# Kernel optimization log

Measured on AMD Instinct MI355X. Metric: run time of the kernel, lower is better.

The kernel has to match this reference:

```python
import jax, jax.numpy as jnp
import numpy as np

N_HEADS = 8
FACTOR = 5


def setup_inputs() -> dict:
    key = jax.random.key(0)
    ks = jax.random.split(key, 8)
    B, L, D = 2, 4096, 512
    sample_k = min(FACTOR * int(np.ceil(np.log(L))), L)  # 45
    inp = {
        "queries": jax.random.normal(ks[0], (B, L, D), jnp.float32),
        "keys": jax.random.normal(ks[1], (B, L, D), jnp.float32),
        "values": jax.random.normal(ks[2], (B, L, D), jnp.float32),
        "Wq": jax.random.normal(ks[3], (D, D), jnp.float32) * 0.02,
        "bq": jnp.zeros((D,), jnp.float32),
        "Wk": jax.random.normal(ks[4], (D, D), jnp.float32) * 0.02,
        "bk": jnp.zeros((D,), jnp.float32),
        "Wv": jax.random.normal(ks[5], (D, D), jnp.float32) * 0.02,
        "bv": jnp.zeros((D,), jnp.float32),
        "index_sample": jax.random.randint(ks[6], (L, sample_k), 0, L, jnp.int32),
    }
    return inp


def reference(queries, keys, values, Wq, bq, Wk, bk, Wv, bv, index_sample):
    b, l_q, d_model = queries.shape
    _, l_k, _ = keys.shape
    h = N_HEADS
    d = d_model // h
    # projections -> [b, h, l, d]
    q = (queries @ Wq + bq).reshape(b, l_q, h, d).transpose(0, 2, 1, 3)
    k = (keys @ Wk + bk).reshape(b, l_k, h, d).transpose(0, 2, 1, 3)
    v = (values @ Wv + bv).reshape(b, l_k, h, d).transpose(0, 2, 1, 3)
    n_top = min(FACTOR * int(np.ceil(np.log(l_q))), l_q)
    # --- prob_qk: sparse sampled QK ---
    # gather sampled keys per query position: [b, h, l_q, sample_k, d]
    k_sample = k[:, :, index_sample, :]
    q_k_sample = jnp.einsum('bhld,bhlsd->bhls', q, k_sample)
    # sparsity measure M(q, K) = max - mean
    m = q_k_sample.max(-1) - q_k_sample.sum(-1) / l_k  # [b, h, l_q]
    _, m_top = jax.lax.top_k(m, n_top)  # [b, h, n_top]
    q_reduce = jnp.take_along_axis(q, m_top[..., None], axis=2)  # [b, h, u, d]
    scores = jnp.einsum('bhud,bhkd->bhuk', q_reduce, k)  # [b, h, u, l_k]
    scale = float(1.0 / np.sqrt(d))
    scores = scores * scale
    # --- causal ProbMask on the selected query rows ---
    causal = jnp.triu(jnp.ones((l_q, l_k), bool), 1)
    mask = causal[m_top]  # [b, h, u, l_k]
    scores = jnp.where(mask, -jnp.inf, scores)
    attn = jax.nn.softmax(scores, axis=-1)
    # --- initial context: causal cumsum of V; scatter updated rows ---
    context = jnp.cumsum(v, axis=2)  # [b, h, l_q, d]
    upd = jnp.einsum('bhuk,bhkd->bhud', attn, v)
    bi = jnp.arange(b)[:, None, None]
    hi = jnp.arange(h)[None, :, None]
    context = context.at[bi, hi, m_top].set(upd)
    return context.transpose(0, 2, 1, 3).reshape(b, l_q, h * d)
```

## Files before the change

### kernel.cpp

```cpp
#include <hip/hip_runtime.h>
#include <math.h>

#define B  2
#define L  4096
#define D  512
#define H  8
#define DH 64
#define BH (B * H)
#define K3 1536
#define XPW 1024

typedef short s16x8 __attribute__((ext_vector_type(8)));
typedef float f32x4 __attribute__((ext_vector_type(4)));

#define AS1 __attribute__((address_space(1)))
#define AS3 __attribute__((address_space(3)))

__device__ __forceinline__ void lds_load16(const void* g, void* l) {
    __builtin_amdgcn_global_load_lds((const AS1 unsigned int*)g,
                                     (AS3 unsigned int*)l, 16, 0, 0);
}

__device__ __forceinline__ unsigned short f2bf(float x) {
    union { float f; unsigned u; } v; v.f = x;
    unsigned u = v.u;
    return (unsigned short)((u + 0x7fff + ((u >> 16) & 1)) >> 16);
}
__device__ __forceinline__ float bf2f(unsigned short h) {
    union { float f; unsigned u; } v; v.u = ((unsigned)h) << 16;
    return v.f;
}

#define MEMFENCE asm volatile("" ::: "memory")
__device__ __forceinline__ void wg_bar() {
    MEMFENCE;
    __builtin_amdgcn_s_barrier();
    MEMFENCE;
}

__global__ __launch_bounds__(256)
void k_split(const float* __restrict__ q, const float* __restrict__ k,
             const float* __restrict__ v,
             const float* __restrict__ wq, const float* __restrict__ wk,
             const float* __restrict__ wv,
             unsigned short* __restrict__ Xp, unsigned short* __restrict__ WpT)
{
    const int tid = threadIdx.x;
    if (blockIdx.x < 192) {
        __shared__ float t[64][65];
        const int bx = blockIdx.x;
        const int e  = bx >> 6;
        const int k0 = (bx & 7) * 64;
        const int n0 = ((bx >> 3) & 7) * 64;
        const float* W = (e == 0) ? wq : (e == 1) ? wk : wv;

        for (int idx = tid; idx < 64 * 16; idx += 256) {
            const int i = idx >> 4, j4 = (idx & 15) << 2;
            *(float4*)&t[i][j4] = *(const float4*)(W + (size_t)(k0 + i) * 512 + n0 + j4);
        }
        __syncthreads();

        const int n_loc = tid >> 2;
        const int kq    = (tid & 3) << 4;
        unsigned short h[16], l[16];
        #pragma unroll
        for (int tt = 0; tt < 16; tt++) {
            const float x = t[kq + tt][n_loc];
            h[tt] = f2bf(x);
            l[tt] = f2bf(x - bf2f(h[tt]));
        }
        unsigned short* base = WpT + (size_t)e * 512 * K3 + (size_t)(n0 + n_loc) * K3 + k0 + kq;
        #pragma unroll
        for (int g4 = 0; g4 < 4; g4++) {
            ushort4 hv = make_ushort4(h[g4*4], h[g4*4+1], h[g4*4+2], h[g4*4+3]);
            ushort4 lv = make_ushort4(l[g4*4], l[g4*4+1], l[g4*4+2], l[g4*4+3]);
            *(ushort4*)(base + g4*4)        = hv;
            *(ushort4*)(base + 512 + g4*4)  = lv;
        }
    } else {
        const size_t g = (size_t)(blockIdx.x - 192) * 256 + tid;
        const size_t per = (size_t)8192 * 128;
        const int e = (int)(g / per);
        const size_t rem = g - (size_t)e * per;
        const int m  = (int)(rem >> 7);
        const int kq = (int)(rem & 127) << 2;

        const float* X = (e == 0) ? q : (e == 1) ? k : v;
        const float4 x = *(const float4*)(X + (size_t)m * 512 + kq);

        unsigned short h0 = f2bf(x.x), h1 = f2bf(x.y), h2 = f2bf(x.z), h3 = f2bf(x.w);
        unsigned short* dst = Xp + (size_t)e * 8192 * XPW + (size_t)m * XPW + kq;
        *(ushort4*)(dst) = make_ushort4(h0, h1, h2, h3);
        if (e != 2) {
            unsigned short l0 = f2bf(x.x - bf2f(h0)), l1 = f2bf(x.y - bf2f(h1));
            unsigned short l2 = f2bf(x.z - bf2f(h2)), l3 = f2bf(x.w - bf2f(h3));
            *(ushort4*)(dst + 512) = make_ushort4(l0, l1, l2, l3);
        }
    }
}

#define MFMA16 __builtin_amdgcn_mfma_f32_16x16x32_bf16

__global__ __launch_bounds__(256, 2)
void gemm_mfma(const unsigned short* __restrict__ Xp,
               const unsigned short* __restrict__ WpT,
               const float* __restrict__ bq, const float* __restrict__ bk,
               const float* __restrict__ bv,
               float* __restrict__ Qo, float* __restrict__ Ko,
               float* __restrict__ Vo)
{
    __shared__ __align__(16) unsigned short lds[32768];

    const int e = blockIdx.z;
    const float* bias = (e == 0) ? bq : (e == 1) ? bk : bv;
    float* C          = (e == 0) ? Qo : (e == 1) ? Ko : Vo;
    const unsigned short* Ag = Xp  + (size_t)e * 8192 * XPW;
    const unsigned short* Bg = WpT + (size_t)e * 512 * K3;

    const int tid  = threadIdx.x;
    const int lane = tid & 63;
    const int wid  = tid >> 6;
    const int wm   = wid & 1;
    const int wn   = wid >> 1;
    const int m0   = blockIdx.x * 128;
    const int n0g  = blockIdx.y * 128;

    const int srow = lane >> 2;
    const int spos = lane & 3;
    const int sswz = (spos ^ ((srow >> 1) & 3)) << 3;
    const int row0 = wid * 32 + srow;
    const int row1 = row0 + 16;

    const unsigned short* aH0 = Ag + (size_t)(m0 + row0) * XPW + sswz;
    const unsigned short* aH1 = Ag + (size_t)(m0 + row1) * XPW + sswz;
    const unsigned short* aL0 = aH0 + 512;
    const unsigned short* aL1 = aH1 + 512;
    const unsigned short* bH0 = Bg + (size_t)(n0g + row0) * K3 + sswz;
    const unsigned short* bH1 = Bg + (size_t)(n0g + row1) * K3 + sswz;
    const unsigned short* bL0 = bH0 + 512;
    const unsigned short* bL1 = bH1 + 512;

    const int wr0 = wid * 1024;
    const int wr1 = wr0 + 512;

    const int r16 = lane & 15, quad = lane >> 4;
    const int laneOff = r16 * 64 + ((quad ^ ((r16 >> 1) & 3)) << 4);
    const char* ldsC = (const char*)lds;

    f32x4 acc[4][4];
    #pragma unroll
    for (int i = 0; i < 4; i++)
        #pragma unroll
        for (int j = 0; j < 4; j++)
            acc[i][j] = (f32x4){0.f, 0.f, 0.f, 0.f};

    const int NT = 16;

    if (e != 2) {
        #define STAGE_QK(kk, nu) do {                                   \
            const int ka_ = (kk) * 32;                                  \
            unsigned short* dd_ = lds + (nu);                           \
            lds_load16(aH0 + ka_, dd_ + wr0);                           \
            lds_load16(aH1 + ka_, dd_ + wr1);                           \
            lds_load16(aL0 + ka_, dd_ + 4096  + wr0);                   \
            lds_load16(aL1 + ka_, dd_ + 4096  + wr1);                   \
            lds_load16(bH0 + ka_, dd_ + 8192  + wr0);                   \
            lds_load16(bH1 + ka_, dd_ + 8192  + wr1);                   \
            lds_load16(bL0 + ka_, dd_ + 12288 + wr0);                   \
            lds_load16(bL1 + ka_, dd_ + 12288 + wr1);                   \
        } while (0)

        STAGE_QK(0, 0);
        s16x8 aF[4], bh[4], bl[4];

        for (int t = 0; t < NT; ++t) {
            const int pa = (t & 1) << 15;
            const int nu = (~t & 1) << 14;
            if (t + 1 < NT) {
                STAGE_QK(t + 1, nu);
                asm volatile("s_waitcnt vmcnt(8)" ::: "memory");
            } else {
                asm volatile("s_waitcnt vmcnt(0)" ::: "memory");
            }
            wg_bar();

            const char* base = ldsC + pa;
            const char* fAh = base + (wm * 64) * 64 + laneOff;
            const char* fAl = base + 8192  + (wm * 64) * 64 + laneOff;
            const char* fBh = base + 16384 + (wn * 64) * 64 + laneOff;
            const char* fBl = base + 24576 + (wn * 64) * 64 + laneOff;

            #pragma unroll
            for (int mq = 0; mq < 4; mq++) aF[mq] = *(const s16x8*)(fAh + mq * 1024);
            #pragma unroll
            for (int nq = 0; nq < 4; nq++) {
                bh[nq] = *(const s16x8*)(fBh + nq * 1024);
                bl[nq] = *(const s16x8*)(fBl + nq * 1024);
            }
            __builtin_amdgcn_s_setprio(1);
            #pragma unroll
            for (int mq = 0; mq < 4; mq++)
                #pragma unroll
                for (int nq = 0; nq < 4; nq++)
                    acc[mq][nq] = MFMA16(aF[mq], bh[nq], acc[mq][nq], 0, 0, 0);
            #pragma unroll
            for (int mq = 0; mq < 4; mq++)
                #pragma unroll
                for (int nq = 0; nq < 4; nq++)
                    acc[mq][nq] = MFMA16(aF[mq], bl[nq], acc[mq][nq], 0, 0, 0);
            __builtin_amdgcn_s_setprio(0);

            #pragma unroll
            for (int mq = 0; mq < 4; mq++) aF[mq] = *(const s16x8*)(fAl + mq * 1024);
            __builtin_amdgcn_s_setprio(1);
            #pragma unroll
            for (int mq = 0; mq < 4; mq++)
                #pragma unroll
                for (int nq = 0; nq < 4; nq++)
                    acc[mq][nq] = MFMA16(aF[mq], bh[nq], acc[mq][nq], 0, 0, 0);
            __builtin_amdgcn_s_setprio(0);
            wg_bar();
        }
    } else {
        #define STAGE_V(kk, nu) do {                                    \
            const int ka_ = (kk) * 32;                                  \
            unsigned short* dd_ = lds + (nu);                           \
            lds_load16(aH0 + ka_, dd_ + wr0);                           \
            lds_load16(aH1 + ka_, dd_ + wr1);                           \
            lds_load16(bH0 + ka_, dd_ + 8192 + wr0);                    \
            lds_load16(bH1 + ka_, dd_ + 8192 + wr1);                    \
        } while (0)

        STAGE_V(0, 0);
        s16x8 aF[4], bh[4];

        for (int t = 0; t < NT; ++t) {
            const int pa = (t & 1) << 15;
            const int nu = (~t & 1) << 14;
            if (t + 1 < NT) {
                STAGE_V(t + 1, nu);
                asm volatile("s_waitcnt vmcnt(4)" ::: "memory");
            } else {
                asm volatile("s_waitcnt vmcnt(0)" ::: "memory");
            }
            wg_bar();

            const char* base = ldsC + pa;
            const char* fAh = base + (wm * 64) * 64 + laneOff;
            const char* fBh = base + 16384 + (wn * 64) * 64 + laneOff;
            #pragma unroll
            for (int mq = 0; mq < 4; mq++) aF[mq] = *(const s16x8*)(fAh + mq * 1024);
            #pragma unroll
            for (int nq = 0; nq < 4; nq++) bh[nq] = *(const s16x8*)(fBh + nq * 1024);
            __builtin_amdgcn_s_setprio(1);
            #pragma unroll
            for (int mq = 0; mq < 4; mq++)
                #pragma unroll
                for (int nq = 0; nq < 4; nq++)
                    acc[mq][nq] = MFMA16(aF[mq], bh[nq], acc[mq][nq], 0, 0, 0);
            __builtin_amdgcn_s_setprio(0);
            wg_bar();
        }
    }

    #pragma unroll
    for (int nt = 0; nt < 4; nt++) {
        const int col = n0g + wn * 64 + nt * 16 + r16;
        const float bb = bias[col];
        #pragma unroll
        for (int mt = 0; mt < 4; mt++) {
            const int row0e = m0 + wm * 64 + mt * 16 + quad * 4;
            #pragma unroll
            for (int i = 0; i < 4; i++)
                C[(size_t)(row0e + i) * 512 + col] = acc[mt][nt][i] + bb;
        }
    }
}

#define CH 64
__global__ __launch_bounds__(256)
void k_sample_chunks(const float* __restrict__ Q, const float* __restrict__ K,
                     const int* __restrict__ idx, float* __restrict__ m_out, int S,
                     const float* __restrict__ V, float* __restrict__ partial)
{
    const int tid = threadIdx.x;
    if (blockIdx.x < 256) {
        const int bid = blockIdx.x;
        const int c  = (bid & 15) * 4 + (tid >> 6);
        const int h  = (bid >> 4) & (H - 1);
        const int b  = bid >> 7;
        const int d  = tid & 63;
        const float* base = V + (size_t)b * L * D + h * DH + d + (size_t)(c * CH) * D;

        float vals[CH];
        #pragma unroll
        for (int i = 0; i < CH; i++) vals[i] = base[(size_t)i * D];

        float s0 = 0.f, s1 = 0.f, s2 = 0.f, s3 = 0.f;
        #pragma unroll
        for (int i = 0; i < CH; i += 4) {
            s0 += vals[i]; s1 += vals[i+1]; s2 += vals[i+2]; s3 += vals[i+3];
        }
        partial[((size_t)((b * H + h) * 64 + c)) * DH + d] = (s0 + s1) + (s2 + s3);
    } else {
        const int lane = tid & 63;
        const int wib  = tid >> 6;
        const int i    = blockIdx.x - 256;
        const int bh   = i & 15;
        const int lg   = i >> 4;
        const int l = lg * 4 + wib;
        const int h = bh & (H - 1);
        const int b = bh >> 3;
        const int widx = (bh << 12) | l;

        const int r4 = lane >> 2;
        const int c4 = lane & 3;

        float4 qf[4];
        {
            const float4* qv = (const float4*)(Q + ((size_t)b * L + l) * D + h * DH);
            #pragma unroll
            for (int ii = 0; ii < 4; ii++) qf[ii] = qv[c4 + 4 * ii];
        }

        const float* Kb = K + (size_t)b * L * D + h * DH;
        const int* is = idx + (size_t)l * S;

        int  jj[3];
        bool ok[3];
        #pragma unroll
        for (int p = 0; p < 3; p++) {
            const int sp = p * 16 + r4;
            ok[p] = sp < S;
            jj[p] = ok[p] ? is[sp] : 0;
        }
        const float4* r0 = (const float4*)(Kb + (size_t)jj[0] * D);
        const float4* r1 = (const float4*)(Kb + (size_t)jj[1] * D);
        const float4* r2 = (const float4*)(Kb + (size_t)jj[2] * D);

        float4 k00 = r0[c4],     k01 = r0[c4 + 4], k02 = r0[c4 + 8], k03 = r0[c4 + 12];
        float4 k10 = r1[c4],     k11 = r1[c4 + 4], k12 = r1[c4 + 8], k13 = r1[c4 + 12];
        float4 k20 = r2[c4],     k21 = r2[c4 + 4], k22 = r2[c4 + 8], k23 = r2[c4 + 12];
        __builtin_amdgcn_sched_barrier(0);

        float vmax = -INFINITY, vsum = 0.f;
        {
            float dot = 0.f;
            dot += qf[0].x * k00.x + qf[0].y * k00.y + qf[0].z * k00.z + qf[0].w * k00.w;
            dot += qf[1].x * k01.x + qf[1].y * k01.y + qf[1].z * k01.z + qf[1].w * k01.w;
            dot += qf[2].x * k02.x + qf[2].y * k02.y + qf[2].z * k02.z + qf[2].w * k02.w;
            dot += qf[3].x * k03.x + qf[3].y * k03.y + qf[3].z * k03.z + qf[3].w * k03.w;
            dot += __shfl_xor(dot, 1, 64);
            dot += __shfl_xor(dot, 2, 64);
            if (ok[0]) { vmax = fmaxf(vmax, dot); if (c4 == 0) vsum += dot; }
        }
        {
            float dot = 0.f;
            dot += qf[0].x * k10.x + qf[0].y * k10.y + qf[0].z * k10.z + qf[0].w * k10.w;
            dot += qf[1].x * k11.x + qf[1].y * k11.y + qf[1].z * k11.z + qf[1].w * k11.w;
            dot += qf[2].x * k12.x + qf[2].y * k12.y + qf[2].z * k12.z + qf[2].w * k12.w;
            dot += qf[3].x * k13.x + qf[3].y * k13.y + qf[3].z * k13.z + qf[3].w * k13.w;
            dot += __shfl_xor(dot, 1, 64);
            dot += __shfl_xor(dot, 2, 64);
            if (ok[1]) { vmax = fmaxf(vmax, dot); if (c4 == 0) vsum += dot; }
        }
        {
            float dot = 0.f;
            dot += qf[0].x * k20.x + qf[0].y * k20.y + qf[0].z * k20.z + qf[0].w * k20.w;
            dot += qf[1].x * k21.x + qf[1].y * k21.y + qf[1].z * k21.z + qf[1].w * k21.w;
            dot += qf[2].x * k22.x + qf[2].y * k22.y + qf[2].z * k22.z + qf[2].w * k22.w;
            dot += qf[3].x * k23.x + qf[3].y * k23.y + qf[3].z * k23.z + qf[3].w * k23.w;
            dot += __shfl_xor(dot, 1, 64);
            dot += __shfl_xor(dot, 2, 64);
            if (ok[2]) { vmax = fmaxf(vmax, dot); if (c4 == 0) vsum += dot; }
        }
        #pragma unroll
        for (int off = 32; off >= 4; off >>= 1) {
            vmax = fmaxf(vmax, __shfl_xor(vmax, off, 64));
            vsum += __shfl_xor(vsum, off, 64);
        }
        if (lane == 0) m_out[widx] = vmax - vsum * (1.0f / (float)L);
    }
}

__global__ __launch_bounds__(256)
void topk_kernel(const float* __restrict__ m_in, int* __restrict__ m_top,
                 float* __restrict__ sums, int* __restrict__ flags, int NT)
{
    __shared__ unsigned hist[256];
    __shared__ unsigned sfx[257];
    __shared__ int sh_b, sh_rem;
    __shared__ int cnt_gt, cnt_eq;
    __shared__ int eqlist[128];

    const float* m = m_in + (size_t)blockIdx.x * L;
    const int tid = threadIdx.x;
    int* out = m_top + blockIdx.x * NT;
    int* fl  = flags + (size_t)blockIdx.x * L;

    if (tid < NT) sums[blockIdx.x * NT + tid] = 0.f;
    for (int i = tid; i < L; i += 256) fl[i] = 0;

    unsigned uv[16];
    #pragma unroll
    for (int k = 0; k < 16; k++) {
        const float f = m[tid + k * 256];
        const unsigned x = __float_as_uint(f);
        uv[k] = (x & 0x80000000u) ? ~x : (x | 0x80000000u);
    }

    unsigned prefix = 0;
    int rem = NT;

    for (int level = 0; level < 4; level++) {
        const int shift = 24 - level * 8;
        hist[tid] = 0;
        if (tid == 0) { cnt_gt = 0; cnt_eq = 0; }
        __syncthreads();
        #pragma unroll
        for (int k = 0; k < 16; k++) {
            const bool part = (level == 0) || ((uv[k] >> (shift + 8)) == prefix);
            if (part) atomicAdd(&hist[(uv[k] >> shift) & 255], 1u);
        }
        __syncthreads();
        if (tid < 64) {
            const unsigned s0 = hist[4*tid+0], s1 = hist[4*tid+1];
            const unsigned s2 = hist[4*tid+2], s3 = hist[4*tid+3];
            const unsigned loc = s0 + s1 + s2 + s3;
            unsigned suf = loc;
            #pragma unroll
            for (int off = 1; off < 64; off <<= 1) {
                const unsigned t = __shfl_down(suf, off, 64);
                if (tid + off < 64) suf += t;
            }
            const unsigned tail = suf - loc;
            sfx[4*tid+3] = tail + s3;
            sfx[4*tid+2] = tail + s3 + s2;
            sfx[4*tid+1] = tail + s3 + s2 + s1;
            sfx[4*tid+0] = suf;
            if (tid == 0) sfx[256] = 0;
        }
        __syncthreads();
        if (sfx[tid + 1] < (unsigned)rem && (unsigned)rem <= sfx[tid]) {
            sh_b   = tid;
            sh_rem = rem - (int)sfx[tid + 1];
        }
        __syncthreads();
        prefix = (prefix << 8) | (unsigned)sh_b;
        rem    = sh_rem;
        __syncthreads();
    }

    const unsigned T = prefix;
    const int n_gt = NT - rem;

    #pragma unroll
    for (int k = 0; k < 16; k++) {
        if (uv[k] > T) {
            const int pos = atomicAdd(&cnt_gt, 1);
            out[pos] = tid + k * 256;
        } else if (uv[k] == T) {
            const int pos = atomicAdd(&cnt_eq, 1);
            if (pos < 128) eqlist[pos] = tid + k * 256;
        }
    }
    __syncthreads();
    if (tid == 0) {
        int n = cnt_eq < 128 ? cnt_eq : 128;
        for (int r = 0; r < rem; r++) {
            int best = 0x7fffffff, bi = 0;
            for (int i = 0; i < n; i++)
                if (eqlist[i] < best) { best = eqlist[i]; bi = i; }
            out[n_gt + r] = best;
            eqlist[bi] = 0x7fffffff;
        }
    }
    __syncthreads();
    if (tid < NT) fl[out[tid]] = 1;
}

__global__ __launch_bounds__(256)
void k_cumsum_scores(const float* __restrict__ V, const float* __restrict__ partial,
                     const int* __restrict__ flags, float* __restrict__ out,
                     const float* __restrict__ Q, const float* __restrict__ K,
                     const int* __restrict__ m_top, float* __restrict__ scores,
                     float* __restrict__ sums, int NT)
{
    const int tid = threadIdx.x;
    if (blockIdx.x < 256) {
        const int bid = blockIdx.x;
        const int c  = (bid & 15) * 4 + (tid >> 6);
        const int h  = (bid >> 4) & (H - 1);
        const int b  = bid >> 7;
        const int d  = tid & 63;
        const size_t off = (size_t)b * L * D + h * DH + d + (size_t)(c * CH) * D;
        const float* base  = V   + off;
        float*       obase = out + off;
        const float* pb = partial + (size_t)((b * H + h) * 64) * DH + d;
        const int*   fp = flags + (size_t)(b * H + h) * L + c * CH;

        float vals[CH];
        #pragma unroll
        for (int i = 0; i < CH; i++) vals[i] = base[(size_t)i * D];

        float acc = 0.f;
        for (int cc = 0; cc < c; cc++) acc += pb[cc * DH];

        #pragma unroll
        for (int i = 0; i < CH; i++) {
            acc += vals[i];
            obase[(size_t)i * D] = fp[i] ? 0.f : acc;
        }
    } else {
        __shared__ float qsh[15][DH];
        __shared__ int   psh[15];

        const int rem2 = blockIdx.x - 256;
        const int bh = rem2 / 24;
        const int r2 = rem2 % 24;
        const int ug = r2 >> 3;
        const int jc = r2 & 7;
        const int h  = bh & (H - 1);
        const int b  = bh >> 3;
        const int j0 = jc * 512;

        for (int i = tid; i < 15 * DH; i += 256) {
            const int u = i >> 6, d = i & 63;
            const int p = m_top[bh * NT + ug * 15 + u];
            if (d == 0) psh[u] = p;
            qsh[u][d] = Q[((size_t)b * L + p) * D + h * DH + d];
        }
        __syncthreads();

        const float* Kb = K + (size_t)b * L * D + h * DH;
        const int ja = j0 + tid;
        const int jb = ja + 256;
        float4 k0[16], k1[16];
        {
            const float4* ra = (const float4*)(Kb + (size_t)ja * D);
            const float4* rb = (const float4*)(Kb + (size_t)jb * D);
            #pragma unroll
            for (int i = 0; i < 16; i++) { k0[i] = ra[i]; k1[i] = rb[i]; }
        }

        for (int u = 0; u < 15; u++) {
            const int p = psh[u];
            const float4* qv = (const float4*)qsh[u];
            float d0 = 0.f, d1 = 0.f;
            #pragma unroll
            for (int i = 0; i < 16; i++) {
                const float4 q4 = qv[i];
                d0 += q4.x * k0[i].x + q4.y * k0[i].y + q4.z * k0[i].z + q4.w * k0[i].w;
                d1 += q4.x * k1[i].x + q4.y * k1[i].y + q4.z * k1[i].z + q4.w * k1[i].w;
            }
            const float e0 = (ja <= p) ? __expf(d0 * 0.125f) : 0.f;
            const float e1 = (jb <= p) ? __expf(d1 * 0.125f) : 0.f;
            float* srow = scores + (size_t)(bh * NT + ug * 15 + u) * L;
            srow[ja] = e0;
            srow[jb] = e1;
            float t = e0 + e1;
            #pragma unroll
            for (int off = 32; off; off >>= 1) t += __shfl_xor(t, off, 64);
            if ((tid & 63) == 0) atomicAdd(&sums[bh * NT + ug * 15 + u], t);
        }
    }
}

__global__ __launch_bounds__(256)
void attn_wv(const float* __restrict__ scores, const float* __restrict__ V,
             const int* __restrict__ m_top, const float* __restrict__ sums,
             float* __restrict__ out, int NT)
{
    __shared__ float ssh[45][64];
    __shared__ float sinv[45];
    __shared__ int   psh[45];

    const int bh = blockIdx.y;
    const int h  = bh & (H - 1);
    const int b  = bh >> 3;
    const int j0 = blockIdx.x * 64;
    const int tid = threadIdx.x;
    const int d   = tid & 63;
    const int w   = tid >> 6;

    if (tid < NT) {
        psh[tid]  = m_top[bh * NT + tid];
        sinv[tid] = 1.0f / sums[bh * NT + tid];
    }

    const float* Vb = V + (size_t)b * L * D + h * DH + d;
    float vreg[64];
    #pragma unroll
    for (int i = 0; i < 64; i++) vreg[i] = Vb[(size_t)(j0 + i) * D];

    __syncthreads();
    for (int i = tid; i < NT * 64; i += 256) {
        const int u = i >> 6, j = i & 63;
        ssh[u][j] = scores[(size_t)(bh * NT + u) * L + j0 + j] * sinv[u];
    }
    __syncthreads();

    for (int u = w; u < NT; u += 4) {
        const int p = psh[u];
        if (p < j0) continue;
        const float* wt = ssh[u];
        float acc = 0.f;
        #pragma unroll
        for (int i = 0; i < 64; i++) acc += wt[i] * vreg[i];
        atomicAdd(out + ((size_t)b * L + p) * D + h * DH + d, acc);
    }
}

extern "C" void kernel_launch(void* const* d_in, const int* in_sizes, int n_in,
                              void* d_out, int out_size, void* d_ws, size_t ws_size,
                              hipStream_t stream)
{
    const float* queries = (const float*)d_in[0];
    const float* keys    = (const float*)d_in[1];
    const float* values  = (const float*)d_in[2];
    const float* Wq      = (const float*)d_in[3];
    const float* bq      = (const float*)d_in[4];
    const float* Wk      = (const float*)d_in[5];
    const float* bk      = (const float*)d_in[6];
    const float* Wv      = (const float*)d_in[7];
    const float* bv      = (const float*)d_in[8];
    const int*   idx     = (const int*)d_in[9];
    float* out = (float*)d_out;

    const int S  = in_sizes[9] / L;
    const int NT = S;

    const size_t NE = (size_t)B * L * D;
    float* Qb      = (float*)d_ws;
    float* Kb      = Qb + NE;
    float* Vb      = Kb + NE;
    float* m_buf   = Vb + NE;
    float* cs_part = m_buf + (size_t)BH * L;
    int*   m_top   = (int*)(cs_part + (size_t)BH * 64 * DH);
    float* sums    = (float*)(m_top + 1024);
    int*   flags   = (int*)(sums + 1024);
    float* scores  = (float*)(flags + (size_t)BH * L);
    unsigned short* Xp  = (unsigned short*)(scores + (size_t)BH * NT * L);
    unsigned short* WpT = Xp + (size_t)3 * 8192 * XPW;

    k_split<<<192 + 3 * 8192 * 128 / 256, 256, 0, stream>>>(
        queries, keys, values, Wq, Wk, Wv, Xp, WpT);

    gemm_mfma<<<dim3(8192 / 128, 512 / 128, 3), 256, 0, stream>>>(
        Xp, WpT, bq, bk, bv, Qb, Kb, Vb);

    k_sample_chunks<<<256 + BH * L / 4, 256, 0, stream>>>(
        Qb, Kb, idx, m_buf, S, Vb, cs_part);

    topk_kernel<<<BH, 256, 0, stream>>>(m_buf, m_top, sums, flags, NT);

    k_cumsum_scores<<<256 + 384, 256, 0, stream>>>(
        Vb, cs_part, flags, out, Qb, Kb, m_top, scores, sums, NT);

    attn_wv<<<dim3(64, BH), 256, 0, stream>>>(scores, Vb, m_top, sums, out, NT);
}
```

Before: 245.4 us.

## Fuse attention-weighted V into score kernel with per-chunk partials and finalize

The score blocks keep their exponentiated scores in shared memory and multiply them by their own 512-key chunk of V. Each block writes partial PV vectors and partial exp-sums per chunk, and a small finalize kernel sums the 8 chunks and normalizes. This drops the global scores round trip, the atomics on sums and output, and the separate attn_wv pass over V. In exchange it uses about 37KB of shared memory per block in the scores path and a heavy per-thread inner loop over 15 rows, which may lower occupancy.

Result: faster. 233.5 us, median of 2 (-4.8%).

```diff
diff --git a/kernel.cpp b/kernel.cpp
--- a/kernel.cpp
+++ b/kernel.cpp
@@ -483,8 +483,8 @@
 void k_cumsum_scores(const float* __restrict__ V, const float* __restrict__ partial,
                      const int* __restrict__ flags, float* __restrict__ out,
                      const float* __restrict__ Q, const float* __restrict__ K,
-                     const int* __restrict__ m_top, float* __restrict__ scores,
-                     float* __restrict__ sums, int NT)
+                     const int* __restrict__ m_top, float* __restrict__ pv_part,
+                     float* __restrict__ esum_part, int NT)
 {
     const int tid = threadIdx.x;
     if (blockIdx.x < 256) {
@@ -514,6 +514,9 @@
     } else {
         __shared__ float qsh[15][DH];
         __shared__ int   psh[15];
+        __shared__ float sE[15][512];
+        __shared__ float sPV[4][15 * 64];
+        __shared__ float sES[15][4];
 
         const int rem2 = blockIdx.x - 256;
         const int bh = rem2 / 24;
@@ -523,6 +526,8 @@
         const int h  = bh & (H - 1);
         const int b  = bh >> 3;
         const int j0 = jc * 512;
+        const int lane = tid & 63;
+        const int w    = tid >> 6;
 
         for (int i = tid; i < 15 * DH; i += 256) {
             const int u = i >> 6, d = i & 63;
@@ -555,60 +560,70 @@
             }
             const float e0 = (ja <= p) ? __expf(d0 * 0.125f) : 0.f;
             const float e1 = (jb <= p) ? __expf(d1 * 0.125f) : 0.f;
-            float* srow = scores + (size_t)(bh * NT + ug * 15 + u) * L;
-            srow[ja] = e0;
-            srow[jb] = e1;
+            sE[u][tid]       = e0;
+            sE[u][tid + 256] = e1;
             float t = e0 + e1;
             #pragma unroll
             for (int off = 32; off; off >>= 1) t += __shfl_xor(t, off, 64);
-            if ((tid & 63) == 0) atomicAdd(&sums[bh * NT + ug * 15 + u], t);
-        }
+            if (lane == 0) sES[u][w] = t;
+        }
+        __syncthreads();
+
+        if (tid < 15)
+            esum_part[((size_t)jc * BH + bh) * NT + ug * 15 + tid] =
+                sES[tid][0] + sES[tid][1] + sES[tid][2] + sES[tid][3];
+
+        const float* Vb = V + (size_t)b * L * D + h * DH + lane;
+        float a[15];
+        #pragma unroll
+        for (int u = 0; u < 15; u++) a[u] = 0.f;
+
+        #pragma unroll
+        for (int ck = 0; ck < 2; ck++) {
+            const int jr = w * 128 + ck * 64;
+            float vreg[64];
+            #pragma unroll
+            for (int i = 0; i < 64; i++)
+                vreg[i] = Vb[(size_t)(j0 + jr + i) * D];
+            #pragma unroll
+            for (int u = 0; u < 15; u++) {
+                float au = a[u];
+                #pragma unroll
+                for (int i = 0; i < 64; i++)
+                    au += sE[u][jr + i] * vreg[i];
+                a[u] = au;
+            }
+        }
+        #pragma unroll
+        for (int u = 0; u < 15; u++) sPV[w][u * 64 + lane] = a[u];
+        __syncthreads();
+
+        float* pvb = pv_part + (((size_t)jc * BH + bh) * NT + (size_t)ug * 15) * 64;
+        for (int i = tid; i < 15 * 64; i += 256)
+            pvb[i] = sPV[0][i] + sPV[1][i] + sPV[2][i] + sPV[3][i];
     }
 }
 
 __global__ __launch_bounds__(256)
-void attn_wv(const float* __restrict__ scores, const float* __restrict__ V,
-             const int* __restrict__ m_top, const float* __restrict__ sums,
-             float* __restrict__ out, int NT)
+void k_finalize(const float* __restrict__ pv_part, const float* __restrict__ esum_part,
+                const int* __restrict__ m_top, float* __restrict__ out, int NT)
 {
-    __shared__ float ssh[45][64];
-    __shared__ float sinv[45];
-    __shared__ int   psh[45];
-
-    const int bh = blockIdx.y;
-    const int h  = bh & (H - 1);
-    const int b  = bh >> 3;
-    const int j0 = blockIdx.x * 64;
     const int tid = threadIdx.x;
-    const int d   = tid & 63;
-    const int w   = tid >> 6;
-
-    if (tid < NT) {
-        psh[tid]  = m_top[bh * NT + tid];
-        sinv[tid] = 1.0f / sums[bh * NT + tid];
-    }
-
-    const float* Vb = V + (size_t)b * L * D + h * DH + d;
-    float vreg[64];
+    const int g = blockIdx.x * 4 + (tid >> 6);
+    if (g >= BH * NT) return;
+    const int d  = tid & 63;
+    const int bh = g / NT;
+    const int u  = g % NT;
+    const int h = bh & (H - 1), b = bh >> 3;
+    const int p = m_top[bh * NT + u];
+
+    float v = 0.f, s = 0.f;
     #pragma unroll
-    for (int i = 0; i < 64; i++) vreg[i] = Vb[(size_t)(j0 + i) * D];
-
-    __syncthreads();
-    for (int i = tid; i < NT * 64; i += 256) {
-        const int u = i >> 6, j = i & 63;
-        ssh[u][j] = scores[(size_t)(bh * NT + u) * L + j0 + j] * sinv[u];
-    }
-    __syncthreads();
-
-    for (int u = w; u < NT; u += 4) {
-        const int p = psh[u];
-        if (p < j0) continue;
-        const float* wt = ssh[u];
-        float acc = 0.f;
-        #pragma unroll
-        for (int i = 0; i < 64; i++) acc += wt[i] * vreg[i];
-        atomicAdd(out + ((size_t)b * L + p) * D + h * DH + d, acc);
-    }
+    for (int js = 0; js < 8; js++) {
+        v += pv_part[(((size_t)js * BH + bh) * NT + u) * 64 + d];
+        s += esum_part[((size_t)js * BH + bh) * NT + u];
+    }
+    out[((size_t)b * L + p) * D + h * DH + d] = v / s;
 }
 
 extern "C" void kernel_launch(void* const* d_in, const int* in_sizes, int n_in,
@@ -639,8 +654,9 @@
     int*   m_top   = (int*)(cs_part + (size_t)BH * 64 * DH);
     float* sums    = (float*)(m_top + 1024);
     int*   flags   = (int*)(sums + 1024);
-    float* scores  = (float*)(flags + (size_t)BH * L);
-    unsigned short* Xp  = (unsigned short*)(scores + (size_t)BH * NT * L);
+    float* pv_part = (float*)(flags + (size_t)BH * L);
+    float* esum_part = pv_part + (size_t)8 * BH * NT * DH;
+    unsigned short* Xp  = (unsigned short*)(pv_part + (size_t)BH * NT * L);
     unsigned short* WpT = Xp + (size_t)3 * 8192 * XPW;
 
     k_split<<<192 + 3 * 8192 * 128 / 256, 256, 0, stream>>>(
@@ -655,7 +671,8 @@
     topk_kernel<<<BH, 256, 0, stream>>>(m_buf, m_top, sums, flags, NT);
 
     k_cumsum_scores<<<256 + 384, 256, 0, stream>>>(
-        Vb, cs_part, flags, out, Qb, Kb, m_top, scores, sums, NT);
-
-    attn_wv<<<dim3(64, BH), 256, 0, stream>>>(scores, Vb, m_top, sums, out, NT);
-}
+        Vb, cs_part, flags, out, Qb, Kb, m_top, pv_part, esum_part, NT);
+
+    k_finalize<<<(BH * NT + 3) / 4, 256, 0, stream>>>(
+        pv_part, esum_part, m_top, out, NT);
+}
```
